# Optimization experiments

Hardware: AMD Instinct MI355X
Metric: run time of the kernel (lower is better)

The kernel has to match this reference:

```python
import jax, jax.numpy as jnp
import numpy as np

HIDDEN_DIM = 64
VOCAB_SIZE = 64
ENTROPY_THRESH = 2.5
SCALE = 1.0 / np.sqrt(HIDDEN_DIM)


def setup_inputs() -> dict:
    key = jax.random.key(0)
    ks = jax.random.split(key, 16)
    B, L, M = 1024, 2048, 256
    H = HIDDEN_DIM
    seq = jax.random.randint(ks[0], (B, L), 0, VOCAB_SIZE, dtype=jnp.int64 if jax.config.jax_enable_x64 else jnp.int32)
    memory = jax.random.normal(ks[1], (B, M, H), dtype=jnp.float32)
    s = 0.05
    params = {
        'embed':  jax.random.normal(ks[2], (VOCAB_SIZE, H)) * s,
        'w_ih':   jax.random.normal(ks[3], (3 * H, 2 * H)) * s,
        'w_hh':   jax.random.normal(ks[4], (3 * H, H)) * s,
        'b_ih':   jax.random.normal(ks[5], (3 * H,)) * s,
        'b_hh':   jax.random.normal(ks[6], (3 * H,)) * s,
        'wq':     jax.random.normal(ks[7], (H, H)) * s,
        'bq':     jax.random.normal(ks[8], (H,)) * s,
        'wk':     jax.random.normal(ks[9], (H, H)) * s,
        'bk':     jax.random.normal(ks[10], (H,)) * s,
        'wv':     jax.random.normal(ks[11], (H, H)) * s,
        'bv':     jax.random.normal(ks[12], (H,)) * s,
        'head_w': jax.random.normal(ks[13], (VOCAB_SIZE, H)) * s,
        'head_b': jax.random.normal(ks[14], (VOCAB_SIZE,)) * s,
    }
    return dict(seq=seq, memory=memory, **params)


def _attention(h, memory, wq, bq, wk, bk, wv, bv):
    # h: [B,H], memory: [B,M,H]
    q = h @ wq.T + bq                                  # [B,H]
    k = jnp.einsum('bmh,oh->bmo', memory, wk) + bk     # [B,M,H]
    v = jnp.einsum('bmh,oh->bmo', memory, wv) + bv     # [B,M,H]
    scores = jnp.einsum('bh,bmh->bm', q, k) * SCALE    # [B,M]
    w = jax.nn.softmax(scores, axis=-1)
    return jnp.einsum('bm,bmh->bh', w, v)              # [B,H]


def _forward(seq, memory, embed, w_ih, w_hh, b_ih, b_hh,
             wq, bq, wk, bk, wv, bv, head_w, head_b):
    B, L = seq.shape
    H = HIDDEN_DIM
    h0 = jnp.zeros((B, H), dtype=memory.dtype)
    r0 = jnp.zeros((B, H), dtype=memory.dtype)

    def step(carry, seq_t):
        h, retrieved, read_count = carry
        x_t = embed[seq_t]                              # [B,H] gather
        inp = jnp.concatenate([x_t, retrieved], axis=-1)  # [B,2H]
        gi = inp @ w_ih.T + b_ih                        # [B,3H]
        gh = h @ w_hh.T + b_hh                          # [B,3H]
        i_r, i_z, i_n = jnp.split(gi, 3, axis=-1)
        h_r, h_z, h_n = jnp.split(gh, 3, axis=-1)
        r = jax.nn.sigmoid(i_r + h_r)
        z = jax.nn.sigmoid(i_z + h_z)
        n = jnp.tanh(i_n + r * h_n)
        h_new = (1.0 - z) * n + z * h
        # entropy gate (no_grad in original)
        logits_t = jax.lax.stop_gradient(h_new @ head_w.T + head_b)
        probs = jax.nn.softmax(logits_t, axis=-1)
        entropy = -(probs * jnp.log(probs + 1e-8)).sum(-1)  # [B]
        cond = entropy.mean() > ENTROPY_THRESH              # scalar bool
        att = _attention(h_new, memory, wq, bq, wk, bk, wv, bv)
        retrieved_new = jnp.where(cond, att, jnp.zeros_like(att))
        return (h_new, retrieved_new, read_count + cond.astype(jnp.int32)), None

    (h, _, read_count), _ = jax.lax.scan(step, (h0, r0, jnp.int32(0)), seq.T)
    logits = h @ head_w.T + head_b
    read_rate = read_count.astype(jnp.float32) / L
    return logits, read_rate


def reference(seq, memory, embed, w_ih, w_hh, b_ih, b_hh,
              wq, bq, wk, bk, wv, bv, head_w, head_b):
    return _forward(seq, memory, embed, w_ih, w_hh, b_ih, b_hh,
                    wq, bq, wk, bk, wv, bv, head_w, head_b)
```

## Files before the change

kernel.cpp:

```cpp
#include <hip/hip_runtime.h>
#include <stdint.h>

#define HD       64
#define MM       256
#define BB       1024
#define LL       2048
#define SCALE_   0.125f
#define GATE_SUM (2560ull << 20)
#define M30      0x3FFFFFFFull
#define M25      0x1FFFFFFull
#define SPIN_FAR 16384
#define SPIN_LDS (1 << 20)

#define WS_RING  0
#define WS_WPA   8192
#define WS_WPB   32768
#define WS_G     57344
#define WS_HWT2  81920
#define WS_W2    98304
#define WS_D     114688
#define WS_E     114944
#define WS_F     115200

#define LD_WPA   0
#define LD_WPB   24576
#define LD_G     49152
#define LD_HWT2  73728
#define LD_DYN   90112
#define DYN_STRIDE 5120
#define DY_GI    0
#define DY_GH    1536
#define DY_H0A   2304
#define DY_H1A   2560
#define DY_H0B   2816
#define DY_H1B   3072
#define DY_NUM   3328
#define DY_WEA   3840
#define DY_WEB   4352
#define DY_SEH   4864
#define LD_MISC  110592

#define P0_W2P   0
#define P0_WVT2  8192
#define P0_D     16384
#define P0_E     16640
#define P0_F     16896
#define P0_MC    17408
#define MC_BYTES 16640

#define LDS_BYTES 150528

__device__ __forceinline__ unsigned bf16r(float x) {
  unsigned u = __float_as_uint(x);
  return (u + 0x7fffu + ((u >> 16) & 1u)) >> 16;
}
__device__ __forceinline__ unsigned pack2(float a, float b) {
  return bf16r(a) | (bf16r(b) << 16);
}
__device__ __forceinline__ float lo16(unsigned u) { return __uint_as_float(u << 16); }
__device__ __forceinline__ float hi16(unsigned u) { return __uint_as_float(u & 0xffff0000u); }

#define WAVE_FENCE() asm volatile("s_waitcnt lgkmcnt(0)" ::: "memory")

extern "C" __global__ void reactive_pre(
    const float* __restrict__ embed, const float* __restrict__ w_ih,
    const float* __restrict__ w_hh,  const float* __restrict__ b_ih,
    const float* __restrict__ wq,    const float* __restrict__ bq,
    const float* __restrict__ wk,    const float* __restrict__ bk,
    const float* __restrict__ head_w, unsigned char* __restrict__ ws)
{
  const int tid = threadIdx.x;

  unsigned* wpa = (unsigned*)(ws + WS_WPA);
  unsigned* wpb = (unsigned*)(ws + WS_WPB);
  for (int i = tid; i < 6144; i += 1024) {
    int q = i / 192, row = i % 192;
    wpa[i] = pack2(w_ih[row * 128 + 64 + 2 * q], w_ih[row * 128 + 64 + 2 * q + 1]);
    wpb[i] = pack2(w_hh[row * 64 + 2 * q],       w_hh[row * 64 + 2 * q + 1]);
  }
  unsigned* gp = (unsigned*)(ws + WS_G);
  for (int i = tid; i < 64 * 96; i += 1024) {
    int v = i / 96, u = i % 96;
    int j0 = 2 * u, j1 = j0 + 1;
    float g0 = b_ih[j0], g1 = b_ih[j1];
    for (int h = 0; h < 64; ++h) {
      float ev = embed[v * 64 + h];
      g0 = fmaf(ev, w_ih[j0 * 128 + h], g0);
      g1 = fmaf(ev, w_ih[j1 * 128 + h], g1);
    }
    gp[i] = pack2(g0, g1);
  }
  float2* hwt2 = (float2*)(ws + WS_HWT2);
  for (int i = tid; i < 2048; i += 1024) {
    int hp = i >> 6, o = i & 63;
    hwt2[i] = make_float2(head_w[o * 64 + 2 * hp], head_w[o * 64 + 2 * hp + 1]);
  }
  float* w2 = (float*)(ws + WS_W2);
  for (int i = tid; i < 4096; i += 1024) {
    int h2 = i >> 6, h = i & 63;
    float a = 0.f;
    for (int o = 0; o < 64; ++o) a = fmaf(wk[o * 64 + h2], wq[o * 64 + h], a);
    w2[i] = a;
  }
  if (tid < 64) {
    float a = 0.f, b2 = 0.f;
    for (int o = 0; o < 64; ++o) a  = fmaf(bk[o], wq[o * 64 + tid], a);
    for (int o = 0; o < 64; ++o) b2 = fmaf(bq[o], wk[o * 64 + tid], b2);
    ((float*)(ws + WS_D))[tid] = a;
    ((float*)(ws + WS_E))[tid] = b2;
  }
  if (tid == 0) {
    float a = 0.f;
    for (int o = 0; o < 64; ++o) a = fmaf(bq[o], bk[o], a);
    *(float*)(ws + WS_F) = a;
  }
}

extern "C" __global__ void __launch_bounds__(512, 2)
reactive_main(const int* __restrict__ seq, const float* __restrict__ memory,
              const float* __restrict__ wvp, const float* __restrict__ bvp,
              const float* __restrict__ b_hh, const float* __restrict__ head_w,
              const float* __restrict__ head_b, unsigned char* __restrict__ ws,
              float* __restrict__ out)
{
  extern __shared__ __align__(16) unsigned char lds[];
  const int tid     = threadIdx.x;
  const int wv      = tid >> 6;
  const int lane    = tid & 63;
  const int half    = wv >> 2;
  const int b_local = wv & 3;
  const int b       = (int)blockIdx.x * 4 + b_local;
  const bool isA    = (half == 0);

  unsigned kp[2][32];
  unsigned vt[64];
  float    cm[2];

  {
    unsigned* w2p  = (unsigned*)(lds + P0_W2P);
    unsigned* wvt2 = (unsigned*)(lds + P0_WVT2);
    float* pD = (float*)(lds + P0_D);
    float* pE = (float*)(lds + P0_E);
    float* pF = (float*)(lds + P0_F);
    const float* wsW2 = (const float*)(ws + WS_W2);
    for (int i = tid; i < 2048; i += 512) {
      int h2 = i >> 5, hp = i & 31;
      w2p[i] = pack2(wsW2[h2 * 64 + 2 * hp], wsW2[h2 * 64 + 2 * hp + 1]);
    }
    for (int i = tid; i < 2048; i += 512) {
      int h2p = i >> 6, l = i & 63;
      wvt2[i] = pack2(wvp[l * 64 + 2 * h2p], wvp[l * 64 + 2 * h2p + 1]);
    }
    if (tid < 64) { pD[tid] = ((const float*)(ws + WS_D))[tid];
                    pE[tid] = ((const float*)(ws + WS_E))[tid]; }
    if (tid == 0) pF[0] = *(const float*)(ws + WS_F);
    __syncthreads();

    float* mc = (float*)(lds + P0_MC + wv * MC_BYTES);
    const float bvl   = bvp[lane];
    const float fscal = pF[0];
    const float* memb = memory + ((size_t)b * MM + (size_t)half * 128) * HD;

    for (int g = 0; g < 2; ++g) {
      WAVE_FENCE();
#pragma unroll 4
      for (int r = 0; r < 64; ++r)
        mc[r * 65 + lane] = memb[(size_t)(g * 64 + r) * HD + lane];
      WAVE_FENCE();

      float acc[64];
#pragma unroll
      for (int h = 0; h < 64; ++h) acc[h] = pD[h];
      float cacc = fscal;
      for (int h2 = 0; h2 < 64; ++h2) {
        float mv = mc[lane * 65 + h2];
        cacc = fmaf(mv, pE[h2], cacc);
        const unsigned* wrow = w2p + h2 * 32;
#pragma unroll
        for (int hp = 0; hp < 32; ++hp) {
          unsigned u = wrow[hp];
          acc[2 * hp]     = fmaf(mv, lo16(u), acc[2 * hp]);
          acc[2 * hp + 1] = fmaf(mv, hi16(u), acc[2 * hp + 1]);
        }
      }
      cm[g] = cacc;
#pragma unroll
      for (int u = 0; u < 32; ++u) kp[g][u] = pack2(acc[2 * u], acc[2 * u + 1]);

      for (int rp = 0; rp < 32; ++rp) {
        float a0 = bvl, a1 = bvl;
#pragma unroll
        for (int hq = 0; hq < 32; ++hq) {
          unsigned w = wvt2[hq * 64 + lane];
          float wl = lo16(w), wh = hi16(w);
          const float2 m0 = *(const float2*)&mc[(2 * rp) * 65 + 2 * hq];
          const float2 m1 = *(const float2*)&mc[(2 * rp + 1) * 65 + 2 * hq];
          a0 = fmaf(m0.x, wl, a0); a0 = fmaf(m0.y, wh, a0);
          a1 = fmaf(m1.x, wl, a1); a1 = fmaf(m1.y, wh, a1);
        }
        vt[32 * g + rp] = pack2(a0, a1);
      }
    }
    __syncthreads();
  }

  {
    const float4* s1 = (const float4*)(ws + WS_WPA);   float4* d1 = (float4*)(lds + LD_WPA);
    for (int i = tid; i < 1536; i += 512) d1[i] = s1[i];
    const float4* s2 = (const float4*)(ws + WS_WPB);   float4* d2 = (float4*)(lds + LD_WPB);
    for (int i = tid; i < 1536; i += 512) d2[i] = s2[i];
    const float4* s3 = (const float4*)(ws + WS_G);     float4* d3 = (float4*)(lds + LD_G);
    for (int i = tid; i < 1536; i += 512) d3[i] = s3[i];
    const float4* s4 = (const float4*)(ws + WS_HWT2);  float4* d4 = (float4*)(lds + LD_HWT2);
    for (int i = tid; i < 1024; i += 512) d4[i] = s4[i];
    float* dz = (float*)(lds + LD_DYN);
    for (int i = tid; i < 4 * DYN_STRIDE / 4; i += 512) dz[i] = 0.f;
    if (tid < 5) ((unsigned*)(lds + LD_MISC))[tid] = 0u;
    __syncthreads();
    if (tid < 4) {
      float* se = (float*)(lds + LD_DYN + tid * DYN_STRIDE + DY_SEH);
      se[0] = 1.f; se[1] = 1.f;
    }
    __syncthreads();
  }

  const unsigned* sWPA = (const unsigned*)(lds + LD_WPA);
  const unsigned* sWPB = (const unsigned*)(lds + LD_WPB);
  const unsigned* sG   = (const unsigned*)(lds + LD_G);
  const float2*   sHW2 = (const float2*)(lds + LD_HWT2);
  unsigned char* dynp = lds + LD_DYN + b_local * DYN_STRIDE;
  float* sGI  = (float*)(dynp + DY_GI);
  float* sGH  = (float*)(dynp + DY_GH);
  float* sH0me = (float*)(dynp + (isA ? DY_H0A : DY_H0B));
  float* sH1me = (float*)(dynp + (isA ? DY_H1A : DY_H1B));
  float* sNUM = (float*)(dynp + DY_NUM);
  float* sWE  = (float*)(dynp + (isA ? DY_WEA : DY_WEB));
  float* sSEH = (float*)(dynp + DY_SEH);
  unsigned long long* sBEC = (unsigned long long*)(lds + LD_MISC);
  volatile unsigned* sCONDW = (volatile unsigned*)(lds + LD_MISC + 16);
  unsigned long long* ring = (unsigned long long*)(ws + WS_RING);
  const int* seqb = seq + (size_t)b * LL;

  float h_reg = 0.f;
  float* hsel_last = sH0me;
  int res_t = 0, rcount = 0;
  bool cprev = false;

  float bh_r = 0.f, bh_z = 0.f, bh_n = 0.f;
  if (!isA) { bh_r = b_hh[lane]; bh_z = b_hh[64 + lane]; bh_n = b_hh[128 + lane]; }
  const float hb_l = head_b[lane];

  float a_gr = 0.f, a_gz = 0.f, a_gn = 0.f, a_dr = 0.f, a_dz = 0.f, a_dn = 0.f;
  float b_hr = 0.f, b_hz = 0.f, b_hn = 0.f;

  for (int t = 0; t < LL; ++t) {
    if (isA) {
      float Se = sSEH[0] + sSEH[1];
      float rcpSe = 1.0f / Se;
      int token = seqb[t];
      float sr = 0.f, sz = 0.f, sn = 0.f;
#pragma unroll
      for (int q = 0; q < 32; ++q) {
        float2 n0 = *(const float2*)&sNUM[2 * q];
        float2 n1 = *(const float2*)&sNUM[64 + 2 * q];
        float a0 = n0.x + n1.x, a1 = n0.y + n1.y;
        unsigned ur = sWPA[q * 192 + lane];
        unsigned uz = sWPA[q * 192 + 64 + lane];
        unsigned un = sWPA[q * 192 + 128 + lane];
        sr = fmaf(a0, lo16(ur), sr); sr = fmaf(a1, hi16(ur), sr);
        sz = fmaf(a0, lo16(uz), sz); sz = fmaf(a1, hi16(uz), sz);
        sn = fmaf(a0, lo16(un), sn); sn = fmaf(a1, hi16(un), sn);
      }
      unsigned gp0 = sG[token * 96 +      (lane >> 1)];
      unsigned gp1 = sG[token * 96 + 32 + (lane >> 1)];
      unsigned gp2 = sG[token * 96 + 64 + (lane >> 1)];
      bool oddl = (lane & 1);
      a_gr = oddl ? hi16(gp0) : lo16(gp0);
      a_gz = oddl ? hi16(gp1) : lo16(gp1);
      a_gn = oddl ? hi16(gp2) : lo16(gp2);
      a_dr = rcpSe * sr; a_dz = rcpSe * sz; a_dn = rcpSe * sn;
      sGI[lane] = a_gr;        sGI[64 + lane] = a_gz;  sGI[128 + lane] = a_gn;
      sGI[192 + lane] = a_dr;  sGI[256 + lane] = a_dz; sGI[320 + lane] = a_dn;
    } else {
      float hr = bh_r, hz = bh_z, hn = bh_n;
      const float* hprev = hsel_last;
#pragma unroll
      for (int q = 0; q < 32; ++q) {
        float2 h01 = *(const float2*)&hprev[2 * q];
        unsigned ur = sWPB[q * 192 + lane];
        unsigned uz = sWPB[q * 192 + 64 + lane];
        unsigned un = sWPB[q * 192 + 128 + lane];
        hr = fmaf(h01.x, lo16(ur), hr); hr = fmaf(h01.y, hi16(ur), hr);
        hz = fmaf(h01.x, lo16(uz), hz); hz = fmaf(h01.y, hi16(uz), hz);
        hn = fmaf(h01.x, lo16(un), hn); hn = fmaf(h01.y, hi16(un), hn);
      }
      b_hr = hr; b_hz = hz; b_hn = hn;
      sGH[lane] = hr; sGH[64 + lane] = hz; sGH[128 + lane] = hn;
    }
    __syncthreads();

    float gi_r, gi_z, gi_n, da_r, da_z, da_n, gh_r, gh_z, gh_n;
    if (isA) {
      gh_r = sGH[lane]; gh_z = sGH[64 + lane]; gh_n = sGH[128 + lane];
      gi_r = a_gr; gi_z = a_gz; gi_n = a_gn; da_r = a_dr; da_z = a_dz; da_n = a_dn;
    } else {
      gi_r = sGI[lane];       gi_z = sGI[64 + lane];  gi_n = sGI[128 + lane];
      da_r = sGI[192 + lane]; da_z = sGI[256 + lane]; da_n = sGI[320 + lane];
      gh_r = b_hr; gh_z = b_hz; gh_n = b_hn;
    }
    float xr0 = gi_r + gh_r, xz0 = gi_z + gh_z;
    float rg0 = 1.f / (1.f + __expf(-xr0));
    float rg1 = 1.f / (1.f + __expf(-(xr0 + da_r)));
    float zg0 = 1.f / (1.f + __expf(-xz0));
    float zg1 = 1.f / (1.f + __expf(-(xz0 + da_z)));
    float na0 = fmaf(rg0, gh_n, gi_n);
    float na1 = fmaf(rg1, gh_n, gi_n + da_n);
    float ee0 = __expf(-2.f * na0), ee1 = __expf(-2.f * na1);
    float n0 = (1.f - ee0) / (1.f + ee0);
    float n1 = (1.f - ee1) / (1.f + ee1);
    float h0 = (1.f - zg0) * n0 + zg0 * h_reg;
    float h1 = (1.f - zg1) * n1 + zg1 * h_reg;
    sH0me[lane] = h0; sH1me[lane] = h1;
    WAVE_FENCE();

    {
      const float* hme = isA ? sH0me : sH1me;
      float lo = hb_l;
#pragma unroll
      for (int hp = 0; hp < 32; ++hp) {
        float2 h01 = *(const float2*)&hme[2 * hp];
        float2 w = sHW2[hp * 64 + lane];
        lo = fmaf(h01.x, w.x, lo); lo = fmaf(h01.y, w.y, lo);
      }
      float pu = __expf(lo);
      float Ss = pu;
#pragma unroll
      for (int off = 32; off; off >>= 1) Ss += __shfl_xor(Ss, off, 64);
      float pr = pu / Ss;
      float ent = pr * __logf(pr + 1e-8f);
#pragma unroll
      for (int off = 32; off; off >>= 1) ent += __shfl_xor(ent, off, 64);
      if (lane == 0) {
        float be = fmaxf(-ent, 0.f);
        unsigned long long fp = (unsigned long long)(unsigned)(be * 1048576.0f + 0.5f);
        unsigned long long add = (1ull << 60) | (isA ? fp : (fp << 30));
        unsigned long long old = atomicAdd(&sBEC[t & 1], add);
        if ((old >> 60) == 7ull) {
          unsigned long long tot = old + add;
          unsigned long long e0s = tot & M30;
          unsigned long long e1s = (tot >> 30) & M30;
          unsigned long long pk = ((unsigned long long)(t + 1) << 50) | (e1s << 25) | e0s;
          __hip_atomic_store(ring + (((size_t)(t & 3)) << 8) + blockIdx.x, pk,
                             __ATOMIC_RELAXED, __HIP_MEMORY_SCOPE_AGENT);
          sBEC[t & 1] = 0ull;
        }
      }
    }

    bool condp = false;
    if (t > 0) {
      if (wv == 0) {
        while (res_t < t) {
          const unsigned long long* rb =
              ring + (((size_t)(res_t & 3)) << 8) + 4 * lane;
          unsigned long long want = (unsigned long long)(res_t + 1);
          unsigned long long v0, v1, v2, v3;
          int guard = SPIN_FAR;
          for (;;) {
            v0 = __hip_atomic_load(rb + 0, __ATOMIC_RELAXED, __HIP_MEMORY_SCOPE_AGENT);
            v1 = __hip_atomic_load(rb + 1, __ATOMIC_RELAXED, __HIP_MEMORY_SCOPE_AGENT);
            v2 = __hip_atomic_load(rb + 2, __ATOMIC_RELAXED, __HIP_MEMORY_SCOPE_AGENT);
            v3 = __hip_atomic_load(rb + 3, __ATOMIC_RELAXED, __HIP_MEMORY_SCOPE_AGENT);
            bool ok = ((v0 >> 50) == want) && ((v1 >> 50) == want) &&
                      ((v2 >> 50) == want) && ((v3 >> 50) == want);
            if (__all(ok)) break;
            if (--guard <= 0) break;
            __builtin_amdgcn_s_sleep(1);
          }
          unsigned long long d;
          if (cprev) d = ((v0 >> 25) & M25) + ((v1 >> 25) & M25) +
                         ((v2 >> 25) & M25) + ((v3 >> 25) & M25);
          else       d = (v0 & M25) + (v1 & M25) + (v2 & M25) + (v3 & M25);
#pragma unroll
          for (int off = 32; off; off >>= 1) d += __shfl_xor(d, off, 64);
          bool c = d > GATE_SUM;
          cprev = c; rcount += c ? 1 : 0;
          ++res_t;
        }
        condp = cprev;
        if (lane == 0) *sCONDW = ((unsigned)(t + 1) << 1) | (condp ? 1u : 0u);
      } else {
        unsigned cv;
        int guard = SPIN_LDS;
        for (;;) {
          cv = *sCONDW;
          if ((cv >> 1) == (unsigned)(t + 1)) break;
          if (--guard <= 0) break;
          __builtin_amdgcn_s_sleep(0);
        }
        condp = ((cv >> 1) == (unsigned)(t + 1)) ? ((cv & 1u) != 0u) : false;
      }
    }
    float h_new = condp ? h1 : h0;
    float* hsel = condp ? sH1me : sH0me;
    hsel_last = hsel;
    h_reg = h_new;

    float s0 = cm[0], s1 = cm[1];
#pragma unroll
    for (int hp = 0; hp < 32; ++hp) {
      float2 h01 = *(const float2*)&hsel[2 * hp];
      unsigned u0 = kp[0][hp], u1 = kp[1][hp];
      s0 = fmaf(h01.x, lo16(u0), s0); s0 = fmaf(h01.y, hi16(u0), s0);
      s1 = fmaf(h01.x, lo16(u1), s1); s1 = fmaf(h01.y, hi16(u1), s1);
    }
    float e0 = __expf(s0 * SCALE_), e1 = __expf(s1 * SCALE_);
    float seh = e0 + e1;
#pragma unroll
    for (int off = 32; off; off >>= 1) seh += __shfl_xor(seh, off, 64);
    sWE[lane] = e0; sWE[64 + lane] = e1;
    if (lane == 0) sSEH[half] = seh;
    WAVE_FENCE();

    float al = 0.f;
    const float4* w4 = (const float4*)sWE;
#pragma unroll
    for (int mp = 0; mp < 32; ++mp) {
      float4 wq4 = w4[mp];
      unsigned u0 = vt[2 * mp], u1 = vt[2 * mp + 1];
      al = fmaf(wq4.x, lo16(u0), al);
      al = fmaf(wq4.y, hi16(u0), al);
      al = fmaf(wq4.z, lo16(u1), al);
      al = fmaf(wq4.w, hi16(u1), al);
    }
    sNUM[half * 64 + lane] = al;
    __syncthreads();
  }

  if (blockIdx.x == 0 && wv == 0) {
    while (res_t < LL) {
      const unsigned long long* rb =
          ring + (((size_t)(res_t & 3)) << 8) + 4 * lane;
      unsigned long long want = (unsigned long long)(res_t + 1);
      unsigned long long v0, v1, v2, v3;
      int guard = SPIN_FAR;
      for (;;) {
        v0 = __hip_atomic_load(rb + 0, __ATOMIC_RELAXED, __HIP_MEMORY_SCOPE_AGENT);
        v1 = __hip_atomic_load(rb + 1, __ATOMIC_RELAXED, __HIP_MEMORY_SCOPE_AGENT);
        v2 = __hip_atomic_load(rb + 2, __ATOMIC_RELAXED, __HIP_MEMORY_SCOPE_AGENT);
        v3 = __hip_atomic_load(rb + 3, __ATOMIC_RELAXED, __HIP_MEMORY_SCOPE_AGENT);
        bool ok = ((v0 >> 50) == want) && ((v1 >> 50) == want) &&
                  ((v2 >> 50) == want) && ((v3 >> 50) == want);
        if (__all(ok)) break;
        if (--guard <= 0) break;
        __builtin_amdgcn_s_sleep(1);
      }
      unsigned long long d;
      if (cprev) d = ((v0 >> 25) & M25) + ((v1 >> 25) & M25) +
                     ((v2 >> 25) & M25) + ((v3 >> 25) & M25);
      else       d = (v0 & M25) + (v1 & M25) + (v2 & M25) + (v3 & M25);
#pragma unroll
      for (int off = 32; off; off >>= 1) d += __shfl_xor(d, off, 64);
      bool c = d > GATE_SUM;
      cprev = c; rcount += c ? 1 : 0;
      ++res_t;
    }
    if (lane == 0) out[BB * 64] = (float)rcount / (float)LL;
  }

  if (isA) {
    float lof = hb_l;
#pragma unroll 8
    for (int h = 0; h < 64; ++h) lof = fmaf(hsel_last[h], head_w[lane * 64 + h], lof);
    out[(size_t)b * 64 + lane] = lof;
  }
}

extern "C" void kernel_launch(void* const* d_in, const int* in_sizes, int n_in,
                              void* d_out, int out_size, void* d_ws, size_t ws_size,
                              hipStream_t stream)
{
  (void)in_sizes; (void)n_in; (void)out_size; (void)ws_size;
  const int*   seq    = (const int*)  d_in[0];
  const float* memory = (const float*)d_in[1];
  const float* embed  = (const float*)d_in[2];
  const float* w_ih   = (const float*)d_in[3];
  const float* w_hh   = (const float*)d_in[4];
  const float* b_ih   = (const float*)d_in[5];
  const float* b_hh   = (const float*)d_in[6];
  const float* wq     = (const float*)d_in[7];
  const float* bq     = (const float*)d_in[8];
  const float* wk     = (const float*)d_in[9];
  const float* bk     = (const float*)d_in[10];
  const float* wv     = (const float*)d_in[11];
  const float* bv     = (const float*)d_in[12];
  const float* head_w = (const float*)d_in[13];
  const float* head_b = (const float*)d_in[14];
  unsigned char* ws   = (unsigned char*)d_ws;
  float* out          = (float*)d_out;

  hipMemsetAsync(d_ws, 0, 8192, stream);

  hipLaunchKernelGGL(reactive_pre, dim3(1), dim3(1024), 0, stream,
                     embed, w_ih, w_hh, b_ih, wq, bq, wk, bk, head_w, ws);

  hipFuncSetAttribute((const void*)reactive_main,
                      hipFuncAttributeMaxDynamicSharedMemorySize, LDS_BYTES);
  hipLaunchKernelGGL(reactive_main, dim3(256), dim3(512), LDS_BYTES, stream,
                     seq, memory, wv, bv, b_hh, head_w, head_b, ws, out);
}
```

Baseline: 21.56 ms.

## Add dedicated polling wave and speculate both gate branches one step deeper

Adds a ninth wave per block that only polls the global ring for the cross-block entropy-gate decision and publishes resolved condition bits to LDS. The ring grows from 4 to 8 slots, and compute waves now evaluate attention for both candidate hidden states (h0 and h1), so the gate resolution can lag further behind the recurrence. The intent is to take the global-memory spin off the critical path of the compute waves. The cost is extra attention arithmetic per step, more LDS use, and a 576-thread block, which may affect occupancy and barrier latency.

```diff
diff --git a/kernel.cpp b/kernel.cpp
--- a/kernel.cpp
+++ b/kernel.cpp
@@ -9,25 +9,25 @@
 #define GATE_SUM (2560ull << 20)
 #define M30      0x3FFFFFFFull
 #define M25      0x1FFFFFFull
-#define SPIN_FAR 16384
-#define SPIN_LDS (1 << 20)
+#define SPIN_FAR (1 << 16)
+#define SPIN_LDS (1 << 22)
 
 #define WS_RING  0
-#define WS_WPA   8192
-#define WS_WPB   32768
-#define WS_G     57344
-#define WS_HWT2  81920
-#define WS_W2    98304
-#define WS_D     114688
-#define WS_E     114944
-#define WS_F     115200
+#define WS_WPA   16384
+#define WS_WPB   40960
+#define WS_G     65536
+#define WS_HWT2  90112
+#define WS_W2    106496
+#define WS_D     122880
+#define WS_E     123136
+#define WS_F     123392
 
 #define LD_WPA   0
 #define LD_WPB   24576
 #define LD_G     49152
 #define LD_HWT2  73728
 #define LD_DYN   90112
-#define DYN_STRIDE 5120
+#define DYN_STRIDE 6656
 #define DY_GI    0
 #define DY_GH    1536
 #define DY_H0A   2304
@@ -35,10 +35,10 @@
 #define DY_H0B   2816
 #define DY_H1B   3072
 #define DY_NUM   3328
-#define DY_WEA   3840
-#define DY_WEB   4352
-#define DY_SEH   4864
-#define LD_MISC  110592
+#define DY_WEA   4352
+#define DY_WEB   5376
+#define DY_SEH   6400
+#define LD_MISC  116736
 
 #define P0_W2P   0
 #define P0_WVT2  8192
@@ -62,6 +62,33 @@
 
 #define WAVE_FENCE() asm volatile("s_waitcnt lgkmcnt(0)" ::: "memory")
 
+__device__ __forceinline__ int try_resolve(const unsigned long long* ring, int s, int lane,
+                                           bool cprev, unsigned long long& dsum, int rounds) {
+  const unsigned long long* rb = ring + (((size_t)(s & 7)) << 8) + 4 * lane;
+  const unsigned long long want = (unsigned long long)(s + 1);
+  unsigned long long v0, v1, v2, v3;
+  int r = 0;
+  for (;;) {
+    v0 = __hip_atomic_load(rb + 0, __ATOMIC_RELAXED, __HIP_MEMORY_SCOPE_AGENT);
+    v1 = __hip_atomic_load(rb + 1, __ATOMIC_RELAXED, __HIP_MEMORY_SCOPE_AGENT);
+    v2 = __hip_atomic_load(rb + 2, __ATOMIC_RELAXED, __HIP_MEMORY_SCOPE_AGENT);
+    v3 = __hip_atomic_load(rb + 3, __ATOMIC_RELAXED, __HIP_MEMORY_SCOPE_AGENT);
+    bool ok = ((v0 >> 50) == want) && ((v1 >> 50) == want) &&
+              ((v2 >> 50) == want) && ((v3 >> 50) == want);
+    if (__all(ok)) break;
+    if (++r >= rounds) return 0;
+    __builtin_amdgcn_s_sleep(2);
+  }
+  unsigned long long d;
+  if (cprev) d = ((v0 >> 25) & M25) + ((v1 >> 25) & M25) +
+                 ((v2 >> 25) & M25) + ((v3 >> 25) & M25);
+  else       d = (v0 & M25) + (v1 & M25) + (v2 & M25) + (v3 & M25);
+#pragma unroll
+  for (int off = 32; off; off >>= 1) d += __shfl_xor(d, off, 64);
+  dsum = d;
+  return 1;
+}
+
 extern "C" __global__ void reactive_pre(
     const float* __restrict__ embed, const float* __restrict__ w_ih,
     const float* __restrict__ w_hh,  const float* __restrict__ b_ih,
@@ -116,7 +143,7 @@
   }
 }
 
-extern "C" __global__ void __launch_bounds__(512, 2)
+extern "C" __global__ void __launch_bounds__(576, 3)
 reactive_main(const int* __restrict__ seq, const float* __restrict__ memory,
               const float* __restrict__ wvp, const float* __restrict__ bvp,
               const float* __restrict__ b_hh, const float* __restrict__ head_w,
@@ -127,10 +154,11 @@
   const int tid     = threadIdx.x;
   const int wv      = tid >> 6;
   const int lane    = tid & 63;
-  const int half    = wv >> 2;
+  const bool isPoll = (wv == 8);
+  const int half    = isPoll ? 0 : (wv >> 2);
   const int b_local = wv & 3;
   const int b       = (int)blockIdx.x * 4 + b_local;
-  const bool isA    = (half == 0);
+  const bool isA    = (!isPoll) && (half == 0);
 
   unsigned kp[2][32];
   unsigned vt[64];
@@ -143,11 +171,11 @@
     float* pE = (float*)(lds + P0_E);
     float* pF = (float*)(lds + P0_F);
     const float* wsW2 = (const float*)(ws + WS_W2);
-    for (int i = tid; i < 2048; i += 512) {
+    for (int i = tid; i < 2048; i += 576) {
       int h2 = i >> 5, hp = i & 31;
       w2p[i] = pack2(wsW2[h2 * 64 + 2 * hp], wsW2[h2 * 64 + 2 * hp + 1]);
     }
-    for (int i = tid; i < 2048; i += 512) {
+    for (int i = tid; i < 2048; i += 576) {
       int h2p = i >> 6, l = i & 63;
       wvt2[i] = pack2(wvp[l * 64 + 2 * h2p], wvp[l * 64 + 2 * h2p + 1]);
     }
@@ -156,49 +184,51 @@
     if (tid == 0) pF[0] = *(const float*)(ws + WS_F);
     __syncthreads();
 
-    float* mc = (float*)(lds + P0_MC + wv * MC_BYTES);
-    const float bvl   = bvp[lane];
-    const float fscal = pF[0];
-    const float* memb = memory + ((size_t)b * MM + (size_t)half * 128) * HD;
-
-    for (int g = 0; g < 2; ++g) {
-      WAVE_FENCE();
+    if (!isPoll) {
+      float* mc = (float*)(lds + P0_MC + wv * MC_BYTES);
+      const float bvl   = bvp[lane];
+      const float fscal = pF[0];
+      const float* memb = memory + ((size_t)b * MM + (size_t)half * 128) * HD;
+
+      for (int g = 0; g < 2; ++g) {
+        WAVE_FENCE();
 #pragma unroll 4
-      for (int r = 0; r < 64; ++r)
-        mc[r * 65 + lane] = memb[(size_t)(g * 64 + r) * HD + lane];
-      WAVE_FENCE();
-
-      float acc[64];
-#pragma unroll
-      for (int h = 0; h < 64; ++h) acc[h] = pD[h];
-      float cacc = fscal;
-      for (int h2 = 0; h2 < 64; ++h2) {
-        float mv = mc[lane * 65 + h2];
-        cacc = fmaf(mv, pE[h2], cacc);
-        const unsigned* wrow = w2p + h2 * 32;
-#pragma unroll
-        for (int hp = 0; hp < 32; ++hp) {
-          unsigned u = wrow[hp];
-          acc[2 * hp]     = fmaf(mv, lo16(u), acc[2 * hp]);
-          acc[2 * hp + 1] = fmaf(mv, hi16(u), acc[2 * hp + 1]);
-        }
-      }
-      cm[g] = cacc;
-#pragma unroll
-      for (int u = 0; u < 32; ++u) kp[g][u] = pack2(acc[2 * u], acc[2 * u + 1]);
-
-      for (int rp = 0; rp < 32; ++rp) {
-        float a0 = bvl, a1 = bvl;
-#pragma unroll
-        for (int hq = 0; hq < 32; ++hq) {
-          unsigned w = wvt2[hq * 64 + lane];
-          float wl = lo16(w), wh = hi16(w);
-          const float2 m0 = *(const float2*)&mc[(2 * rp) * 65 + 2 * hq];
-          const float2 m1 = *(const float2*)&mc[(2 * rp + 1) * 65 + 2 * hq];
-          a0 = fmaf(m0.x, wl, a0); a0 = fmaf(m0.y, wh, a0);
-          a1 = fmaf(m1.x, wl, a1); a1 = fmaf(m1.y, wh, a1);
-        }
-        vt[32 * g + rp] = pack2(a0, a1);
+        for (int r = 0; r < 64; ++r)
+          mc[r * 65 + lane] = memb[(size_t)(g * 64 + r) * HD + lane];
+        WAVE_FENCE();
+
+        float acc[64];
+#pragma unroll
+        for (int h = 0; h < 64; ++h) acc[h] = pD[h];
+        float cacc = fscal;
+        for (int h2 = 0; h2 < 64; ++h2) {
+          float mv = mc[lane * 65 + h2];
+          cacc = fmaf(mv, pE[h2], cacc);
+          const unsigned* wrow = w2p + h2 * 32;
+#pragma unroll
+          for (int hp = 0; hp < 32; ++hp) {
+            unsigned u = wrow[hp];
+            acc[2 * hp]     = fmaf(mv, lo16(u), acc[2 * hp]);
+            acc[2 * hp + 1] = fmaf(mv, hi16(u), acc[2 * hp + 1]);
+          }
+        }
+        cm[g] = cacc;
+#pragma unroll
+        for (int u = 0; u < 32; ++u) kp[g][u] = pack2(acc[2 * u], acc[2 * u + 1]);
+
+        for (int rp = 0; rp < 32; ++rp) {
+          float a0 = bvl, a1 = bvl;
+#pragma unroll
+          for (int hq = 0; hq < 32; ++hq) {
+            unsigned w = wvt2[hq * 64 + lane];
+            float wl = lo16(w), wh = hi16(w);
+            const float2 m0 = *(const float2*)&mc[(2 * rp) * 65 + 2 * hq];
+            const float2 m1 = *(const float2*)&mc[(2 * rp + 1) * 65 + 2 * hq];
+            a0 = fmaf(m0.x, wl, a0); a0 = fmaf(m0.y, wh, a0);
+            a1 = fmaf(m1.x, wl, a1); a1 = fmaf(m1.y, wh, a1);
+          }
+          vt[32 * g + rp] = pack2(a0, a1);
+        }
       }
     }
     __syncthreads();
@@ -206,20 +236,20 @@
 
   {
     const float4* s1 = (const float4*)(ws + WS_WPA);   float4* d1 = (float4*)(lds + LD_WPA);
-    for (int i = tid; i < 1536; i += 512) d1[i] = s1[i];
+    for (int i = tid; i < 1536; i += 576) d1[i] = s1[i];
     const float4* s2 = (const float4*)(ws + WS_WPB);   float4* d2 = (float4*)(lds + LD_WPB);
-    for (int i = tid; i < 1536; i += 512) d2[i] = s2[i];
+    for (int i = tid; i < 1536; i += 576) d2[i] = s2[i];
     const float4* s3 = (const float4*)(ws + WS_G);     float4* d3 = (float4*)(lds + LD_G);
-    for (int i = tid; i < 1536; i += 512) d3[i] = s3[i];
+    for (int i = tid; i < 1536; i += 576) d3[i] = s3[i];
     const float4* s4 = (const float4*)(ws + WS_HWT2);  float4* d4 = (float4*)(lds + LD_HWT2);
-    for (int i = tid; i < 1024; i += 512) d4[i] = s4[i];
+    for (int i = tid; i < 1024; i += 576) d4[i] = s4[i];
     float* dz = (float*)(lds + LD_DYN);
-    for (int i = tid; i < 4 * DYN_STRIDE / 4; i += 512) dz[i] = 0.f;
+    for (int i = tid; i < 4 * DYN_STRIDE / 4; i += 576) dz[i] = 0.f;
     if (tid < 5) ((unsigned*)(lds + LD_MISC))[tid] = 0u;
     __syncthreads();
     if (tid < 4) {
-      float* se = (float*)(lds + LD_DYN + tid * DYN_STRIDE + DY_SEH);
-      se[0] = 1.f; se[1] = 1.f;
+      float* se = (float*)(lds + LD_DYN + (tid & 3) * DYN_STRIDE + DY_SEH);
+      se[0] = 1.f; se[1] = 1.f; se[2] = 1.f; se[3] = 1.f;
     }
     __syncthreads();
   }
@@ -229,249 +259,250 @@
   const unsigned* sG   = (const unsigned*)(lds + LD_G);
   const float2*   sHW2 = (const float2*)(lds + LD_HWT2);
   unsigned char* dynp = lds + LD_DYN + b_local * DYN_STRIDE;
-  float* sGI  = (float*)(dynp + DY_GI);
-  float* sGH  = (float*)(dynp + DY_GH);
+  float* sGI   = (float*)(dynp + DY_GI);
+  float* sGH   = (float*)(dynp + DY_GH);
   float* sH0me = (float*)(dynp + (isA ? DY_H0A : DY_H0B));
   float* sH1me = (float*)(dynp + (isA ? DY_H1A : DY_H1B));
-  float* sNUM = (float*)(dynp + DY_NUM);
-  float* sWE  = (float*)(dynp + (isA ? DY_WEA : DY_WEB));
-  float* sSEH = (float*)(dynp + DY_SEH);
+  float* sNUM  = (float*)(dynp + DY_NUM);
+  float* sWE   = (float*)(dynp + (isA ? DY_WEA : DY_WEB));
+  float* sSEH  = (float*)(dynp + DY_SEH);
   unsigned long long* sBEC = (unsigned long long*)(lds + LD_MISC);
   volatile unsigned* sCONDW = (volatile unsigned*)(lds + LD_MISC + 16);
   unsigned long long* ring = (unsigned long long*)(ws + WS_RING);
   const int* seqb = seq + (size_t)b * LL;
 
-  float h_reg = 0.f;
-  float* hsel_last = sH0me;
-  int res_t = 0, rcount = 0;
+  float h0_reg = 0.f, h1_reg = 0.f;
+  int cnt = 0, rc = 0;
+  unsigned bits = 0;
   bool cprev = false;
 
   float bh_r = 0.f, bh_z = 0.f, bh_n = 0.f;
-  if (!isA) { bh_r = b_hh[lane]; bh_z = b_hh[64 + lane]; bh_n = b_hh[128 + lane]; }
+  if (!isPoll && !isA) { bh_r = b_hh[lane]; bh_z = b_hh[64 + lane]; bh_n = b_hh[128 + lane]; }
   const float hb_l = head_b[lane];
 
   float a_gr = 0.f, a_gz = 0.f, a_gn = 0.f, a_dr = 0.f, a_dz = 0.f, a_dn = 0.f;
   float b_hr = 0.f, b_hz = 0.f, b_hn = 0.f;
+  float h_reg = 0.f;
 
   for (int t = 0; t < LL; ++t) {
-    if (isA) {
-      float Se = sSEH[0] + sSEH[1];
-      float rcpSe = 1.0f / Se;
-      int token = seqb[t];
-      float sr = 0.f, sz = 0.f, sn = 0.f;
-#pragma unroll
-      for (int q = 0; q < 32; ++q) {
-        float2 n0 = *(const float2*)&sNUM[2 * q];
-        float2 n1 = *(const float2*)&sNUM[64 + 2 * q];
-        float a0 = n0.x + n1.x, a1 = n0.y + n1.y;
-        unsigned ur = sWPA[q * 192 + lane];
-        unsigned uz = sWPA[q * 192 + 64 + lane];
-        unsigned un = sWPA[q * 192 + 128 + lane];
-        sr = fmaf(a0, lo16(ur), sr); sr = fmaf(a1, hi16(ur), sr);
-        sz = fmaf(a0, lo16(uz), sz); sz = fmaf(a1, hi16(uz), sz);
-        sn = fmaf(a0, lo16(un), sn); sn = fmaf(a1, hi16(un), sn);
-      }
-      unsigned gp0 = sG[token * 96 +      (lane >> 1)];
-      unsigned gp1 = sG[token * 96 + 32 + (lane >> 1)];
-      unsigned gp2 = sG[token * 96 + 64 + (lane >> 1)];
-      bool oddl = (lane & 1);
-      a_gr = oddl ? hi16(gp0) : lo16(gp0);
-      a_gz = oddl ? hi16(gp1) : lo16(gp1);
-      a_gn = oddl ? hi16(gp2) : lo16(gp2);
-      a_dr = rcpSe * sr; a_dz = rcpSe * sz; a_dn = rcpSe * sn;
-      sGI[lane] = a_gr;        sGI[64 + lane] = a_gz;  sGI[128 + lane] = a_gn;
-      sGI[192 + lane] = a_dr;  sGI[256 + lane] = a_dz; sGI[320 + lane] = a_dn;
+    if (isPoll) {
+      while (cnt < t - 1) {
+        unsigned long long ds;
+        if (!try_resolve(ring, cnt, lane, cprev, ds, SPIN_FAR)) ds = 0;
+        cprev = ds > GATE_SUM; rc += cprev ? 1 : 0;
+        bits = (bits << 1) | (cprev ? 1u : 0u); ++cnt;
+        if (lane == 0) *sCONDW = ((unsigned)cnt << 8) | (bits & 0xFFu);
+      }
+      if (cnt < t) {
+        unsigned long long ds;
+        if (try_resolve(ring, cnt, lane, cprev, ds, 6)) {
+          cprev = ds > GATE_SUM; rc += cprev ? 1 : 0;
+          bits = (bits << 1) | (cprev ? 1u : 0u); ++cnt;
+          if (lane == 0) *sCONDW = ((unsigned)cnt << 8) | (bits & 0xFFu);
+        }
+      }
     } else {
-      float hr = bh_r, hz = bh_z, hn = bh_n;
-      const float* hprev = hsel_last;
-#pragma unroll
-      for (int q = 0; q < 32; ++q) {
-        float2 h01 = *(const float2*)&hprev[2 * q];
-        unsigned ur = sWPB[q * 192 + lane];
-        unsigned uz = sWPB[q * 192 + 64 + lane];
-        unsigned un = sWPB[q * 192 + 128 + lane];
-        hr = fmaf(h01.x, lo16(ur), hr); hr = fmaf(h01.y, hi16(ur), hr);
-        hz = fmaf(h01.x, lo16(uz), hz); hz = fmaf(h01.y, hi16(uz), hz);
-        hn = fmaf(h01.x, lo16(un), hn); hn = fmaf(h01.y, hi16(un), hn);
-      }
-      b_hr = hr; b_hz = hz; b_hn = hn;
-      sGH[lane] = hr; sGH[64 + lane] = hz; sGH[128 + lane] = hn;
-    }
-    __syncthreads();
-
-    float gi_r, gi_z, gi_n, da_r, da_z, da_n, gh_r, gh_z, gh_n;
-    if (isA) {
-      gh_r = sGH[lane]; gh_z = sGH[64 + lane]; gh_n = sGH[128 + lane];
-      gi_r = a_gr; gi_z = a_gz; gi_n = a_gn; da_r = a_dr; da_z = a_dz; da_n = a_dn;
-    } else {
-      gi_r = sGI[lane];       gi_z = sGI[64 + lane];  gi_n = sGI[128 + lane];
-      da_r = sGI[192 + lane]; da_z = sGI[256 + lane]; da_n = sGI[320 + lane];
-      gh_r = b_hr; gh_z = b_hz; gh_n = b_hn;
-    }
-    float xr0 = gi_r + gh_r, xz0 = gi_z + gh_z;
-    float rg0 = 1.f / (1.f + __expf(-xr0));
-    float rg1 = 1.f / (1.f + __expf(-(xr0 + da_r)));
-    float zg0 = 1.f / (1.f + __expf(-xz0));
-    float zg1 = 1.f / (1.f + __expf(-(xz0 + da_z)));
-    float na0 = fmaf(rg0, gh_n, gi_n);
-    float na1 = fmaf(rg1, gh_n, gi_n + da_n);
-    float ee0 = __expf(-2.f * na0), ee1 = __expf(-2.f * na1);
-    float n0 = (1.f - ee0) / (1.f + ee0);
-    float n1 = (1.f - ee1) / (1.f + ee1);
-    float h0 = (1.f - zg0) * n0 + zg0 * h_reg;
-    float h1 = (1.f - zg1) * n1 + zg1 * h_reg;
-    sH0me[lane] = h0; sH1me[lane] = h1;
-    WAVE_FENCE();
-
-    {
-      const float* hme = isA ? sH0me : sH1me;
-      float lo = hb_l;
-#pragma unroll
-      for (int hp = 0; hp < 32; ++hp) {
-        float2 h01 = *(const float2*)&hme[2 * hp];
-        float2 w = sHW2[hp * 64 + lane];
-        lo = fmaf(h01.x, w.x, lo); lo = fmaf(h01.y, w.y, lo);
-      }
-      float pu = __expf(lo);
-      float Ss = pu;
-#pragma unroll
-      for (int off = 32; off; off >>= 1) Ss += __shfl_xor(Ss, off, 64);
-      float pr = pu / Ss;
-      float ent = pr * __logf(pr + 1e-8f);
-#pragma unroll
-      for (int off = 32; off; off >>= 1) ent += __shfl_xor(ent, off, 64);
-      if (lane == 0) {
-        float be = fmaxf(-ent, 0.f);
-        unsigned long long fp = (unsigned long long)(unsigned)(be * 1048576.0f + 0.5f);
-        unsigned long long add = (1ull << 60) | (isA ? fp : (fp << 30));
-        unsigned long long old = atomicAdd(&sBEC[t & 1], add);
-        if ((old >> 60) == 7ull) {
-          unsigned long long tot = old + add;
-          unsigned long long e0s = tot & M30;
-          unsigned long long e1s = (tot >> 30) & M30;
-          unsigned long long pk = ((unsigned long long)(t + 1) << 50) | (e1s << 25) | e0s;
-          __hip_atomic_store(ring + (((size_t)(t & 3)) << 8) + blockIdx.x, pk,
-                             __ATOMIC_RELAXED, __HIP_MEMORY_SCOPE_AGENT);
-          sBEC[t & 1] = 0ull;
-        }
-      }
-    }
-
-    bool condp = false;
-    if (t > 0) {
-      if (wv == 0) {
-        while (res_t < t) {
-          const unsigned long long* rb =
-              ring + (((size_t)(res_t & 3)) << 8) + 4 * lane;
-          unsigned long long want = (unsigned long long)(res_t + 1);
-          unsigned long long v0, v1, v2, v3;
-          int guard = SPIN_FAR;
-          for (;;) {
-            v0 = __hip_atomic_load(rb + 0, __ATOMIC_RELAXED, __HIP_MEMORY_SCOPE_AGENT);
-            v1 = __hip_atomic_load(rb + 1, __ATOMIC_RELAXED, __HIP_MEMORY_SCOPE_AGENT);
-            v2 = __hip_atomic_load(rb + 2, __ATOMIC_RELAXED, __HIP_MEMORY_SCOPE_AGENT);
-            v3 = __hip_atomic_load(rb + 3, __ATOMIC_RELAXED, __HIP_MEMORY_SCOPE_AGENT);
-            bool ok = ((v0 >> 50) == want) && ((v1 >> 50) == want) &&
-                      ((v2 >> 50) == want) && ((v3 >> 50) == want);
-            if (__all(ok)) break;
-            if (--guard <= 0) break;
-            __builtin_amdgcn_s_sleep(1);
-          }
-          unsigned long long d;
-          if (cprev) d = ((v0 >> 25) & M25) + ((v1 >> 25) & M25) +
-                         ((v2 >> 25) & M25) + ((v3 >> 25) & M25);
-          else       d = (v0 & M25) + (v1 & M25) + (v2 & M25) + (v3 & M25);
-#pragma unroll
-          for (int off = 32; off; off >>= 1) d += __shfl_xor(d, off, 64);
-          bool c = d > GATE_SUM;
-          cprev = c; rcount += c ? 1 : 0;
-          ++res_t;
-        }
-        condp = cprev;
-        if (lane == 0) *sCONDW = ((unsigned)(t + 1) << 1) | (condp ? 1u : 0u);
-      } else {
-        unsigned cv;
-        int guard = SPIN_LDS;
+      bool c2 = false;
+      if (t >= 2) {
+        unsigned cv; int guard = SPIN_LDS;
         for (;;) {
           cv = *sCONDW;
-          if ((cv >> 1) == (unsigned)(t + 1)) break;
+          if ((int)(cv >> 8) >= t - 1) break;
           if (--guard <= 0) break;
           __builtin_amdgcn_s_sleep(0);
         }
-        condp = ((cv >> 1) == (unsigned)(t + 1)) ? ((cv & 1u) != 0u) : false;
-      }
-    }
-    float h_new = condp ? h1 : h0;
-    float* hsel = condp ? sH1me : sH0me;
-    hsel_last = hsel;
-    h_reg = h_new;
-
-    float s0 = cm[0], s1 = cm[1];
-#pragma unroll
-    for (int hp = 0; hp < 32; ++hp) {
-      float2 h01 = *(const float2*)&hsel[2 * hp];
-      unsigned u0 = kp[0][hp], u1 = kp[1][hp];
-      s0 = fmaf(h01.x, lo16(u0), s0); s0 = fmaf(h01.y, hi16(u0), s0);
-      s1 = fmaf(h01.x, lo16(u1), s1); s1 = fmaf(h01.y, hi16(u1), s1);
-    }
-    float e0 = __expf(s0 * SCALE_), e1 = __expf(s1 * SCALE_);
-    float seh = e0 + e1;
-#pragma unroll
-    for (int off = 32; off; off >>= 1) seh += __shfl_xor(seh, off, 64);
-    sWE[lane] = e0; sWE[64 + lane] = e1;
-    if (lane == 0) sSEH[half] = seh;
-    WAVE_FENCE();
-
-    float al = 0.f;
-    const float4* w4 = (const float4*)sWE;
-#pragma unroll
-    for (int mp = 0; mp < 32; ++mp) {
-      float4 wq4 = w4[mp];
-      unsigned u0 = vt[2 * mp], u1 = vt[2 * mp + 1];
-      al = fmaf(wq4.x, lo16(u0), al);
-      al = fmaf(wq4.y, hi16(u0), al);
-      al = fmaf(wq4.z, lo16(u1), al);
-      al = fmaf(wq4.w, hi16(u1), al);
-    }
-    sNUM[half * 64 + lane] = al;
+        int off = (int)(cv >> 8) - (t - 1);
+        c2 = (off >= 0 && off < 8) ? (((cv >> off) & 1u) != 0u) : false;
+      }
+      h_reg = c2 ? h1_reg : h0_reg;
+
+      if (isA) {
+        float Se = sSEH[c2 ? 2 : 0] + sSEH[c2 ? 3 : 1];
+        float rcpSe = 1.0f / Se;
+        const float* nm = sNUM + (c2 ? 128 : 0);
+        int token = seqb[t];
+        float sr = 0.f, sz = 0.f, sn = 0.f;
+#pragma unroll
+        for (int q = 0; q < 32; ++q) {
+          float2 n0 = *(const float2*)&nm[2 * q];
+          float2 n1 = *(const float2*)&nm[64 + 2 * q];
+          float a0 = n0.x + n1.x, a1 = n0.y + n1.y;
+          unsigned ur = sWPA[q * 192 + lane];
+          unsigned uz = sWPA[q * 192 + 64 + lane];
+          unsigned un = sWPA[q * 192 + 128 + lane];
+          sr = fmaf(a0, lo16(ur), sr); sr = fmaf(a1, hi16(ur), sr);
+          sz = fmaf(a0, lo16(uz), sz); sz = fmaf(a1, hi16(uz), sz);
+          sn = fmaf(a0, lo16(un), sn); sn = fmaf(a1, hi16(un), sn);
+        }
+        unsigned gp0 = sG[token * 96 +      (lane >> 1)];
+        unsigned gp1 = sG[token * 96 + 32 + (lane >> 1)];
+        unsigned gp2 = sG[token * 96 + 64 + (lane >> 1)];
+        bool oddl = (lane & 1);
+        a_gr = oddl ? hi16(gp0) : lo16(gp0);
+        a_gz = oddl ? hi16(gp1) : lo16(gp1);
+        a_gn = oddl ? hi16(gp2) : lo16(gp2);
+        a_dr = rcpSe * sr; a_dz = rcpSe * sz; a_dn = rcpSe * sn;
+        sGI[lane] = a_gr;        sGI[64 + lane] = a_gz;  sGI[128 + lane] = a_gn;
+        sGI[192 + lane] = a_dr;  sGI[256 + lane] = a_dz; sGI[320 + lane] = a_dn;
+      } else {
+        const float* hprev = c2 ? sH1me : sH0me;
+        float hr = bh_r, hz = bh_z, hn = bh_n;
+#pragma unroll
+        for (int q = 0; q < 32; ++q) {
+          float2 h01 = *(const float2*)&hprev[2 * q];
+          unsigned ur = sWPB[q * 192 + lane];
+          unsigned uz = sWPB[q * 192 + 64 + lane];
+          unsigned un = sWPB[q * 192 + 128 + lane];
+          hr = fmaf(h01.x, lo16(ur), hr); hr = fmaf(h01.y, hi16(ur), hr);
+          hz = fmaf(h01.x, lo16(uz), hz); hz = fmaf(h01.y, hi16(uz), hz);
+          hn = fmaf(h01.x, lo16(un), hn); hn = fmaf(h01.y, hi16(un), hn);
+        }
+        b_hr = hr; b_hz = hz; b_hn = hn;
+        sGH[lane] = hr; sGH[64 + lane] = hz; sGH[128 + lane] = hn;
+      }
+    }
     __syncthreads();
-  }
-
-  if (blockIdx.x == 0 && wv == 0) {
-    while (res_t < LL) {
-      const unsigned long long* rb =
-          ring + (((size_t)(res_t & 3)) << 8) + 4 * lane;
-      unsigned long long want = (unsigned long long)(res_t + 1);
-      unsigned long long v0, v1, v2, v3;
-      int guard = SPIN_FAR;
-      for (;;) {
-        v0 = __hip_atomic_load(rb + 0, __ATOMIC_RELAXED, __HIP_MEMORY_SCOPE_AGENT);
-        v1 = __hip_atomic_load(rb + 1, __ATOMIC_RELAXED, __HIP_MEMORY_SCOPE_AGENT);
-        v2 = __hip_atomic_load(rb + 2, __ATOMIC_RELAXED, __HIP_MEMORY_SCOPE_AGENT);
-        v3 = __hip_atomic_load(rb + 3, __ATOMIC_RELAXED, __HIP_MEMORY_SCOPE_AGENT);
-        bool ok = ((v0 >> 50) == want) && ((v1 >> 50) == want) &&
-                  ((v2 >> 50) == want) && ((v3 >> 50) == want);
-        if (__all(ok)) break;
-        if (--guard <= 0) break;
-        __builtin_amdgcn_s_sleep(1);
-      }
-      unsigned long long d;
-      if (cprev) d = ((v0 >> 25) & M25) + ((v1 >> 25) & M25) +
-                     ((v2 >> 25) & M25) + ((v3 >> 25) & M25);
-      else       d = (v0 & M25) + (v1 & M25) + (v2 & M25) + (v3 & M25);
-#pragma unroll
-      for (int off = 32; off; off >>= 1) d += __shfl_xor(d, off, 64);
-      bool c = d > GATE_SUM;
-      cprev = c; rcount += c ? 1 : 0;
-      ++res_t;
-    }
-    if (lane == 0) out[BB * 64] = (float)rcount / (float)LL;
+
+    if (isPoll) {
+      while (cnt <= t) {
+        unsigned long long ds;
+        if (!try_resolve(ring, cnt, lane, cprev, ds, 6)) break;
+        cprev = ds > GATE_SUM; rc += cprev ? 1 : 0;
+        bits = (bits << 1) | (cprev ? 1u : 0u); ++cnt;
+        if (lane == 0) *sCONDW = ((unsigned)cnt << 8) | (bits & 0xFFu);
+      }
+    } else {
+      float gi_r, gi_z, gi_n, da_r, da_z, da_n, gh_r, gh_z, gh_n;
+      if (isA) {
+        gh_r = sGH[lane]; gh_z = sGH[64 + lane]; gh_n = sGH[128 + lane];
+        gi_r = a_gr; gi_z = a_gz; gi_n = a_gn; da_r = a_dr; da_z = a_dz; da_n = a_dn;
+      } else {
+        gi_r = sGI[lane];       gi_z = sGI[64 + lane];  gi_n = sGI[128 + lane];
+        da_r = sGI[192 + lane]; da_z = sGI[256 + lane]; da_n = sGI[320 + lane];
+        gh_r = b_hr; gh_z = b_hz; gh_n = b_hn;
+      }
+      float xr0 = gi_r + gh_r, xz0 = gi_z + gh_z;
+      float rg0 = 1.f / (1.f + __expf(-xr0));
+      float rg1 = 1.f / (1.f + __expf(-(xr0 + da_r)));
+      float zg0 = 1.f / (1.f + __expf(-xz0));
+      float zg1 = 1.f / (1.f + __expf(-(xz0 + da_z)));
+      float na0 = fmaf(rg0, gh_n, gi_n);
+      float na1 = fmaf(rg1, gh_n, gi_n + da_n);
+      float ee0 = __expf(-2.f * na0), ee1 = __expf(-2.f * na1);
+      float n0 = (1.f - ee0) / (1.f + ee0);
+      float n1 = (1.f - ee1) / (1.f + ee1);
+      float h0 = (1.f - zg0) * n0 + zg0 * h_reg;
+      float h1 = (1.f - zg1) * n1 + zg1 * h_reg;
+      h0_reg = h0; h1_reg = h1;
+      sH0me[lane] = h0; sH1me[lane] = h1;
+      WAVE_FENCE();
+
+      {
+        const float* hme = isA ? sH0me : sH1me;
+        float lo = hb_l;
+#pragma unroll
+        for (int hp = 0; hp < 32; ++hp) {
+          float2 h01 = *(const float2*)&hme[2 * hp];
+          float2 w = sHW2[hp * 64 + lane];
+          lo = fmaf(h01.x, w.x, lo); lo = fmaf(h01.y, w.y, lo);
+        }
+        float pu = __expf(lo);
+        float Ss = pu;
+#pragma unroll
+        for (int off = 32; off; off >>= 1) Ss += __shfl_xor(Ss, off, 64);
+        float pr = pu / Ss;
+        float ent = pr * __logf(pr + 1e-8f);
+#pragma unroll
+        for (int off = 32; off; off >>= 1) ent += __shfl_xor(ent, off, 64);
+        if (lane == 0) {
+          float be = fmaxf(-ent, 0.f);
+          unsigned long long fp = (unsigned long long)(unsigned)(be * 1048576.0f + 0.5f);
+          unsigned long long add = (1ull << 60) | (isA ? fp : (fp << 30));
+          unsigned long long old = atomicAdd(&sBEC[t & 1], add);
+          if ((old >> 60) == 7ull) {
+            unsigned long long tot = old + add;
+            unsigned long long e0s = tot & M30;
+            unsigned long long e1s = (tot >> 30) & M30;
+            unsigned long long pk = ((unsigned long long)(t + 1) << 50) | (e1s << 25) | e0s;
+            __hip_atomic_store(ring + (((size_t)(t & 7)) << 8) + blockIdx.x, pk,
+                               __ATOMIC_RELAXED, __HIP_MEMORY_SCOPE_AGENT);
+            sBEC[t & 1] = 0ull;
+          }
+        }
+      }
+
+      {
+        float s00 = cm[0], s01 = cm[1], s10 = cm[0], s11 = cm[1];
+        const float2* h02 = (const float2*)sH0me;
+        const float2* h12 = (const float2*)sH1me;
+#pragma unroll
+        for (int hp = 0; hp < 32; ++hp) {
+          float2 ha = h02[hp], hb = h12[hp];
+          unsigned u0 = kp[0][hp], u1 = kp[1][hp];
+          float l0 = lo16(u0), g0 = hi16(u0), l1 = lo16(u1), g1 = hi16(u1);
+          s00 = fmaf(ha.x, l0, s00); s00 = fmaf(ha.y, g0, s00);
+          s01 = fmaf(ha.x, l1, s01); s01 = fmaf(ha.y, g1, s01);
+          s10 = fmaf(hb.x, l0, s10); s10 = fmaf(hb.y, g0, s10);
+          s11 = fmaf(hb.x, l1, s11); s11 = fmaf(hb.y, g1, s11);
+        }
+        float e00 = __expf(s00 * SCALE_), e01 = __expf(s01 * SCALE_);
+        float e10 = __expf(s10 * SCALE_), e11 = __expf(s11 * SCALE_);
+        float sa = e00 + e01, sb = e10 + e11;
+#pragma unroll
+        for (int off = 32; off; off >>= 1) {
+          sa += __shfl_xor(sa, off, 64);
+          sb += __shfl_xor(sb, off, 64);
+        }
+        sWE[lane] = e00; sWE[64 + lane] = e01;
+        sWE[128 + lane] = e10; sWE[192 + lane] = e11;
+        if (lane == 0) { sSEH[half] = sa; sSEH[2 + half] = sb; }
+        WAVE_FENCE();
+
+        float al0 = 0.f, al1 = 0.f;
+        const float4* wa = (const float4*)sWE;
+        const float4* wb = (const float4*)(sWE + 128);
+#pragma unroll
+        for (int mp = 0; mp < 32; ++mp) {
+          float4 qa = wa[mp], qb = wb[mp];
+          unsigned u0 = vt[2 * mp], u1 = vt[2 * mp + 1];
+          float v0 = lo16(u0), v1 = hi16(u0), v2 = lo16(u1), v3 = hi16(u1);
+          al0 = fmaf(qa.x, v0, al0); al0 = fmaf(qa.y, v1, al0);
+          al0 = fmaf(qa.z, v2, al0); al0 = fmaf(qa.w, v3, al0);
+          al1 = fmaf(qb.x, v0, al1); al1 = fmaf(qb.y, v1, al1);
+          al1 = fmaf(qb.z, v2, al1); al1 = fmaf(qb.w, v3, al1);
+        }
+        sNUM[half * 64 + lane] = al0;
+        sNUM[128 + half * 64 + lane] = al1;
+      }
+    }
+    __syncthreads();
+  }
+
+  if (isPoll) {
+    while (cnt < LL) {
+      unsigned long long ds;
+      if (!try_resolve(ring, cnt, lane, cprev, ds, SPIN_FAR)) ds = 0;
+      cprev = ds > GATE_SUM; rc += cprev ? 1 : 0;
+      bits = (bits << 1) | (cprev ? 1u : 0u); ++cnt;
+      if (lane == 0) *sCONDW = ((unsigned)cnt << 8) | (bits & 0xFFu);
+    }
+    if (blockIdx.x == 0 && lane == 0) out[BB * 64] = (float)rc / (float)LL;
   }
 
   if (isA) {
+    unsigned cv; int guard = SPIN_LDS;
+    for (;;) {
+      cv = *sCONDW;
+      if ((int)(cv >> 8) >= LL - 1) break;
+      if (--guard <= 0) break;
+      __builtin_amdgcn_s_sleep(1);
+    }
+    int off = (int)(cv >> 8) - (LL - 1);
+    bool c = (off >= 0 && off < 8) ? (((cv >> off) & 1u) != 0u) : false;
+    const float* hf = c ? sH1me : sH0me;
     float lof = hb_l;
 #pragma unroll 8
-    for (int h = 0; h < 64; ++h) lof = fmaf(hsel_last[h], head_w[lane * 64 + h], lof);
+    for (int h = 0; h < 64; ++h) lof = fmaf(hf[h], head_w[lane * 64 + h], lof);
     out[(size_t)b * 64 + lane] = lof;
   }
 }
@@ -499,13 +530,13 @@
   unsigned char* ws   = (unsigned char*)d_ws;
   float* out          = (float*)d_out;
 
-  hipMemsetAsync(d_ws, 0, 8192, stream);
+  hipMemsetAsync(d_ws, 0, 16384, stream);
 
   hipLaunchKernelGGL(reactive_pre, dim3(1), dim3(1024), 0, stream,
                      embed, w_ih, w_hh, b_ih, wq, bq, wk, bk, head_w, ws);
 
   hipFuncSetAttribute((const void*)reactive_main,
                       hipFuncAttributeMaxDynamicSharedMemorySize, LDS_BYTES);
-  hipLaunchKernelGGL(reactive_main, dim3(256), dim3(512), LDS_BYTES, stream,
+  hipLaunchKernelGGL(reactive_main, dim3(256), dim3(576), LDS_BYTES, stream,
                      seq, memory, wv, bv, b_hh, head_w, head_b, ws, out);
 }
```

Result: slower. 31.30 ms (+45.2%).
